# Performance work log

Measured on AMD Instinct MI355X. Metric: run time of the kernel, lower is better.

## Reference

```python
import jax, jax.numpy as jnp
import numpy as np

N_HEADS = 16
D_HEAD = 64
QUERY_DIM = 1024
CONTEXT_DIM = 1024
INNER = N_HEADS * D_HEAD


def setup_inputs() -> dict:
    key = jax.random.key(0)
    ks = jax.random.split(key, 7)
    B, Nq, Nk = 4, 1024, 1024
    x = jax.random.normal(ks[0], (B, Nq, QUERY_DIM), dtype=jnp.float32)
    context = jax.random.normal(ks[1], (B, Nk, CONTEXT_DIM), dtype=jnp.float32)
    s_q = 1.0 / np.sqrt(QUERY_DIM)
    s_c = 1.0 / np.sqrt(CONTEXT_DIM)
    s_i = 1.0 / np.sqrt(INNER)
    Wq = jax.random.uniform(ks[2], (QUERY_DIM, INNER), jnp.float32, -s_q, s_q)
    Wk = jax.random.uniform(ks[3], (CONTEXT_DIM, INNER), jnp.float32, -s_c, s_c)
    Wv = jax.random.uniform(ks[4], (CONTEXT_DIM, INNER), jnp.float32, -s_c, s_c)
    Wo = jax.random.uniform(ks[5], (INNER, QUERY_DIM), jnp.float32, -s_i, s_i)
    bo = jax.random.uniform(ks[6], (QUERY_DIM,), jnp.float32, -s_i, s_i)
    return {"x": x, "context": context, "Wq": Wq, "Wk": Wk, "Wv": Wv, "Wo": Wo, "bo": bo}


def reference(x, context, Wq, Wk, Wv, Wo, bo):
    B, Nq, _ = x.shape
    Nk = context.shape[1]
    scale = D_HEAD ** -0.5
    # project and split heads: [B, H, N, d]
    q = (x @ Wq).reshape(B, Nq, N_HEADS, D_HEAD).transpose(0, 2, 1, 3)
    k = (context @ Wk).reshape(B, Nk, N_HEADS, D_HEAD).transpose(0, 2, 1, 3)
    v = (context @ Wv).reshape(B, Nk, N_HEADS, D_HEAD).transpose(0, 2, 1, 3)
    scores = jnp.einsum("bhqd,bhkd->bhqk", q, k) * scale
    attn = jax.nn.softmax(scores, axis=-1)
    out = jnp.einsum("bhqk,bhkd->bhqd", attn, v)
    out = out.transpose(0, 2, 1, 3).reshape(B, Nq, INNER)
    return out @ Wo + bo
```

## Files before the change

### kernel.cpp

```cpp
#include <hip/hip_runtime.h>
#include <hip/hip_bf16.h>

#define BATCH 4
#define NQ 1024
#define NKK 1024
#define HD 1024
#define NHEADS 16

typedef __bf16 bf16x8 __attribute__((ext_vector_type(8)));
typedef float f32x4 __attribute__((ext_vector_type(4)));
typedef unsigned short u16;
typedef unsigned short u16x8 __attribute__((ext_vector_type(8)));
typedef unsigned int u32;

__device__ __forceinline__ u16 f2bf(float f) {
    union { __bf16 h; u16 u; } v;
    v.h = (__bf16)f;
    return v.u;
}

#define GLOAD16(gp, lp) \
    __builtin_amdgcn_global_load_lds((const __attribute__((address_space(1))) void*)(gp), \
                                     (__attribute__((address_space(3))) void*)(lp), 16, 0, 0)

#define MFMA16(a, b, c) __builtin_amdgcn_mfma_f32_16x16x32_bf16(a, b, c, 0, 0, 0)

__global__ __launch_bounds__(256) void prep_k(const float* __restrict__ x,
                                              const float* __restrict__ ctx,
                                              const float* __restrict__ w0,
                                              const float* __restrict__ w1,
                                              const float* __restrict__ w2,
                                              const float* __restrict__ w3,
                                              u16* __restrict__ ws,
                                              u16* __restrict__ Xb,
                                              u16* __restrict__ Cb) {
    const int tid = threadIdx.x;
    const int z = blockIdx.z;
    if (z >= 4) {
        const float* src = (z == 4) ? x : ctx;
        u16* dst = (z == 4) ? Xb : Cb;
        const int seg = blockIdx.y * 16 + blockIdx.x;
#pragma unroll
        for (int p = 0; p < 16; ++p) {
            const int i = seg * 4096 + p * 256 + tid;
            float4 v = ((const float4*)src)[i];
            ushort4 pk;
            pk.x = f2bf(v.x); pk.y = f2bf(v.y); pk.z = f2bf(v.z); pk.w = f2bf(v.w);
            ((ushort4*)dst)[i] = pk;
        }
        return;
    }
    const float* src = z == 0 ? w0 : z == 1 ? w1 : z == 2 ? w2 : w3;
    const float scl = (z == 0) ? 0.18033688011112042f : 1.0f;
    u16* dst = ws + (size_t)z * (1024u * 1024u);
    __shared__ u16 t[64][65];
    const int bx = blockIdx.x * 64;
    const int by = blockIdx.y * 64;
#pragma unroll
    for (int p = 0; p < 16; ++p) {
        int idx = p * 256 + tid;
        int r = idx >> 6, c = idx & 63;
        t[c][r] = f2bf(scl * src[(size_t)(by + r) * 1024 + bx + c]);
    }
    __syncthreads();
#pragma unroll
    for (int p = 0; p < 16; ++p) {
        int idx = p * 256 + tid;
        int r = idx >> 6, c = idx & 63;
        dst[(size_t)(bx + r) * 1024 + by + c] = t[r][c];
    }
}

__global__ __launch_bounds__(512) void gemm_qkv(const u16* __restrict__ Xb,
                                                const u16* __restrict__ Cb,
                                                const u16* __restrict__ WqT,
                                                const u16* __restrict__ WkT,
                                                const u16* __restrict__ WvT,
                                                u16* __restrict__ Qb,
                                                u16* __restrict__ Kb,
                                                u16* __restrict__ VTb) {
    const int bid = blockIdx.x;
    const int swz = (bid & 7) * 96 + (bid >> 3);
    const int z = swz >> 8;
    const int rem = swz & 255;
    const int m0 = (rem >> 3) * 128;
    const int n0 = (rem & 7) * 128;

    const u16* __restrict__ A  = (z == 0) ? Xb : Cb;
    const u16* __restrict__ BT = (z == 0) ? WqT : (z == 1) ? WkT : WvT;

    __shared__ __align__(16) u16 Asm[128 * 64];
    __shared__ __align__(16) u16 Bsm[128 * 64];

    const int tid = threadIdx.x, lane = tid & 63, wv = tid >> 6;
    const int wm = wv >> 2, wn = wv & 3;
    const int lr = lane & 15, lg = lane >> 4;
    const int lx = lr & 7;
    const int M = BATCH * NQ, N = HD, K = HD;

    f32x4 acc[4][2];
#pragma unroll
    for (int i = 0; i < 4; ++i)
#pragma unroll
        for (int j = 0; j < 2; ++j) acc[i][j] = (f32x4)(0.0f);

    for (int kt = 0; kt < K; kt += 64) {
        __syncthreads();
#pragma unroll
        for (int i = 0; i < 2; ++i) {
            const int cb = (wv * 2 + i) * 64;
            const int s = cb + lane;
            const int row = s >> 3, cg = (s & 7) ^ (row & 7);
            GLOAD16(A + (size_t)(m0 + row) * K + kt + cg * 8, &Asm[cb * 8]);
            GLOAD16(BT + (size_t)(n0 + row) * K + kt + cg * 8, &Bsm[cb * 8]);
        }
        __syncthreads();
        bf16x8 af[4][2], bfr[2][2];
#pragma unroll
        for (int m = 0; m < 4; ++m)
#pragma unroll
            for (int kk = 0; kk < 2; ++kk)
                af[m][kk] = *(const bf16x8*)&Asm[((wm * 64 + m * 16 + lr) * 8 +
                                                 ((kk * 4 + lg) ^ lx)) * 8];
#pragma unroll
        for (int n = 0; n < 2; ++n)
#pragma unroll
            for (int kk = 0; kk < 2; ++kk)
                bfr[n][kk] = *(const bf16x8*)&Bsm[((wn * 32 + n * 16 + lr) * 8 +
                                                  ((kk * 4 + lg) ^ lx)) * 8];
#pragma unroll
        for (int kk = 0; kk < 2; ++kk)
#pragma unroll
            for (int m = 0; m < 4; ++m)
#pragma unroll
                for (int n = 0; n < 2; ++n)
                    acc[m][n] = MFMA16(af[m][kk], bfr[n][kk], acc[m][n]);
    }

    if (z < 2) {
        u16* __restrict__ C = (z == 0) ? Qb : Kb;
#pragma unroll
        for (int m = 0; m < 4; ++m)
#pragma unroll
            for (int n = 0; n < 2; ++n) {
                const int col = n0 + wn * 32 + n * 16 + lr;
                const int rb = m0 + wm * 64 + m * 16 + lg * 4;
#pragma unroll
                for (int r = 0; r < 4; ++r)
                    C[(size_t)(rb + r) * N + col] = f2bf(acc[m][n][r]);
            }
    } else {
#pragma unroll
        for (int m = 0; m < 4; ++m)
#pragma unroll
            for (int n = 0; n < 2; ++n) {
                const int col = n0 + wn * 32 + n * 16 + lr;
                const int rb = m0 + wm * 64 + m * 16 + lg * 4;
                ushort4 pk;
                pk.x = f2bf(acc[m][n][0]);
                pk.y = f2bf(acc[m][n][1]);
                pk.z = f2bf(acc[m][n][2]);
                pk.w = f2bf(acc[m][n][3]);
                *(ushort4*)&VTb[(size_t)col * M + rb] = pk;
            }
    }
}

__global__ __launch_bounds__(512) void gemm_out(const u16* __restrict__ A,
                                                const u16* __restrict__ BT,
                                                const float* __restrict__ bias,
                                                float* __restrict__ C) {
    const int bid = blockIdx.x;
    const int swz = (bid & 7) * 32 + (bid >> 3);
    const int m0 = (swz >> 3) * 128;
    const int n0 = (swz & 7) * 128;

    __shared__ __align__(16) u16 Asm[128 * 64];
    __shared__ __align__(16) u16 Bsm[128 * 64];

    const int tid = threadIdx.x, lane = tid & 63, wv = tid >> 6;
    const int wm = wv >> 2, wn = wv & 3;
    const int lr = lane & 15, lg = lane >> 4;
    const int lx = lr & 7;
    const int N = HD, K = HD;

    f32x4 acc[4][2];
#pragma unroll
    for (int i = 0; i < 4; ++i)
#pragma unroll
        for (int j = 0; j < 2; ++j) acc[i][j] = (f32x4)(0.0f);

    for (int kt = 0; kt < K; kt += 64) {
        __syncthreads();
#pragma unroll
        for (int i = 0; i < 2; ++i) {
            const int cb = (wv * 2 + i) * 64;
            const int s = cb + lane;
            const int row = s >> 3, cg = (s & 7) ^ (row & 7);
            GLOAD16(A + (size_t)(m0 + row) * K + kt + cg * 8, &Asm[cb * 8]);
            GLOAD16(BT + (size_t)(n0 + row) * K + kt + cg * 8, &Bsm[cb * 8]);
        }
        __syncthreads();
        bf16x8 af[4][2], bfr[2][2];
#pragma unroll
        for (int m = 0; m < 4; ++m)
#pragma unroll
            for (int kk = 0; kk < 2; ++kk)
                af[m][kk] = *(const bf16x8*)&Asm[((wm * 64 + m * 16 + lr) * 8 +
                                                 ((kk * 4 + lg) ^ lx)) * 8];
#pragma unroll
        for (int n = 0; n < 2; ++n)
#pragma unroll
            for (int kk = 0; kk < 2; ++kk)
                bfr[n][kk] = *(const bf16x8*)&Bsm[((wn * 32 + n * 16 + lr) * 8 +
                                                  ((kk * 4 + lg) ^ lx)) * 8];
#pragma unroll
        for (int kk = 0; kk < 2; ++kk)
#pragma unroll
            for (int m = 0; m < 4; ++m)
#pragma unroll
                for (int n = 0; n < 2; ++n)
                    acc[m][n] = MFMA16(af[m][kk], bfr[n][kk], acc[m][n]);
    }

#pragma unroll
    for (int m = 0; m < 4; ++m)
#pragma unroll
        for (int n = 0; n < 2; ++n) {
            const int col = n0 + wn * 32 + n * 16 + lr;
            const int rb = m0 + wm * 64 + m * 16 + lg * 4;
            const float bv = bias[col];
#pragma unroll
            for (int r = 0; r < 4; ++r)
                C[(size_t)(rb + r) * N + col] = acc[m][n][r] + bv;
        }
}

__global__ __launch_bounds__(256) void attn_k(const u16* __restrict__ Q,
                                              const u16* __restrict__ Kp,
                                              const u16* __restrict__ VT,
                                              u16* __restrict__ AO) {
    __shared__ __align__(16) u16 Ksm[2][64 * 64];
    __shared__ __align__(16) u16 Vsm[2][64 * 64];
    __shared__ __align__(16) u16 Psm[4][16 * 64];

    const int tid = threadIdx.x, lane = tid & 63, wv = tid >> 6;
    const int lr = lane & 15, lg = lane >> 4;

    const int swz = (blockIdx.x & 7) * 128 + (blockIdx.x >> 3);
    const int bh = swz >> 4;
    const int b = bh >> 4, h = bh & 15;
    const int q0 = (swz & 15) * 64 + wv * 16;
    const int lx = lr & 7;

    bf16x8 qf[2];
#pragma unroll
    for (int ks = 0; ks < 2; ++ks)
        qf[ks] = *(const bf16x8*)&Q[(size_t)(b * NQ + q0 + lr) * HD +
                                    h * 64 + ks * 32 + lg * 8];

    bf16x8 onesf;
#pragma unroll
    for (int i = 0; i < 8; ++i) onesf[i] = (__bf16)1.0f;

    const int kbase = b * NKK, vrow0 = h * 64;
    auto stageKV = [&](int kt, int bufsel) {
#pragma unroll
        for (int i = 0; i < 2; ++i) {
            const int cb = (wv * 2 + i) * 64;
            const int s = cb + lane;
            const int row = s >> 3;
            const int cg = (s & 7) ^ (row & 7);
            GLOAD16(Kp + (size_t)(kbase + kt + row) * HD + h * 64 + cg * 8,
                    &Ksm[bufsel][cb * 8]);
            GLOAD16(VT + (size_t)(vrow0 + row) * (BATCH * NKK) + kbase + kt + cg * 8,
                    &Vsm[bufsel][cb * 8]);
        }
    };

    f32x4 osum = (f32x4)(0.0f);
    f32x4 o[4];
#pragma unroll
    for (int n = 0; n < 4; ++n) o[n] = (f32x4)(0.0f);

    stageKV(0, 0);
    __syncthreads();
    int cur = 0;

    for (int t = 0; t < NKK / 64; ++t) {
        if (t + 1 < NKK / 64) stageKV((t + 1) * 64, cur ^ 1);
        const u16* Ks = &Ksm[cur][0];
        const u16* Vs = &Vsm[cur][0];

        f32x4 s[4];
#pragma unroll
        for (int n = 0; n < 4; ++n) s[n] = (f32x4)(0.0f);
        __builtin_amdgcn_s_setprio(1);
#pragma unroll
        for (int n = 0; n < 4; ++n) {
            bf16x8 kf0 = *(const bf16x8*)&Ks[(n * 16 + lr) * 64 + (lg ^ lx) * 8];
            bf16x8 kf1 = *(const bf16x8*)&Ks[(n * 16 + lr) * 64 + ((lg | 4) ^ lx) * 8];
            s[n] = MFMA16(kf0, qf[0], s[n]);
            s[n] = MFMA16(kf1, qf[1], s[n]);
        }
        __builtin_amdgcn_s_setprio(0);

        u16* P = &Psm[wv][0];
#pragma unroll
        for (int n = 0; n < 4; ++n) {
            const float p0 = exp2f(s[n][0]);
            const float p1 = exp2f(s[n][1]);
            const float p2 = exp2f(s[n][2]);
            const float p3 = exp2f(s[n][3]);
            ushort4 pk;
            pk.x = f2bf(p0); pk.y = f2bf(p1); pk.z = f2bf(p2); pk.w = f2bf(p3);
            const int ch = (2 * n + (lg >> 1)) ^ lx;
            *(ushort4*)&P[lr * 64 + ch * 8 + (lg & 1) * 4] = pk;
        }

#pragma unroll
        for (int ks = 0; ks < 2; ++ks) {
            bf16x8 pa = *(const bf16x8*)&P[lr * 64 + (((ks * 4 + lg) ^ lx)) * 8];
            __builtin_amdgcn_s_setprio(1);
#pragma unroll
            for (int n = 0; n < 4; ++n) {
                bf16x8 vf = *(const bf16x8*)&Vs[(n * 16 + lr) * 64 + (((ks * 4 + lg) ^ lx)) * 8];
                o[n] = MFMA16(pa, vf, o[n]);
            }
            osum = MFMA16(pa, onesf, osum);
            __builtin_amdgcn_s_setprio(0);
        }
        __syncthreads();
        cur ^= 1;
    }

    float rs[4];
#pragma unroll
    for (int r = 0; r < 4; ++r) rs[r] = 1.0f / osum[r];

#pragma unroll
    for (int n = 0; n < 4; ++n)
#pragma unroll
        for (int r = 0; r < 4; ++r) {
            const float val = o[n][r] * rs[r];
            AO[(size_t)(b * NQ + q0 + lg * 4 + r) * HD +
               h * 64 + n * 16 + lr] = f2bf(val);
        }
}

extern "C" void kernel_launch(void* const* d_in, const int* in_sizes, int n_in,
                              void* d_out, int out_size, void* d_ws, size_t ws_size,
                              hipStream_t stream) {
    const float* x   = (const float*)d_in[0];
    const float* ctx = (const float*)d_in[1];
    const float* Wq  = (const float*)d_in[2];
    const float* Wk  = (const float*)d_in[3];
    const float* Wv  = (const float*)d_in[4];
    const float* Wo  = (const float*)d_in[5];
    const float* bo  = (const float*)d_in[6];

    u16* ws = (u16*)d_ws;
    const size_t MEG = 1024u * 1024u;
    u16* WqT = ws + 0 * MEG;
    u16* WkT = ws + 1 * MEG;
    u16* WvT = ws + 2 * MEG;
    u16* WoT = ws + 3 * MEG;
    u16* Xb  = ws + 4 * MEG;
    u16* Cb  = ws + 8 * MEG;
    u16* Qb  = ws + 12 * MEG;
    u16* Kb  = ws + 16 * MEG;
    u16* VTb = ws + 20 * MEG;
    u16* AOb = Xb;

    prep_k<<<dim3(16, 16, 6), 256, 0, stream>>>(x, ctx, Wq, Wk, Wv, Wo, ws, Xb, Cb);
    gemm_qkv<<<768, 512, 0, stream>>>(Xb, Cb, WqT, WkT, WvT, Qb, Kb, VTb);
    attn_k<<<1024, 256, 0, stream>>>(Qb, Kb, VTb, AOb);
    gemm_out<<<256, 512, 0, stream>>>(AOb, WoT, bo, (float*)d_out);
}
```

Measured before the change: 99.56 us.

## Rewrite QKV GEMM as 256x256 double-buffered pipelined kernel with interleaved loads

Replaces the 128x128 single-buffered QKV projection GEMM with a 256x256 tile kernel that keeps two K-stages in 128KB of dynamic LDS. Global-to-LDS loads for upcoming stages are split into halves and issued between MFMA phases, using explicit vmcnt waits, scheduling barriers and setprio. The three weight matrices are treated as one concatenated 3072-column B operand. The aim is to raise arithmetic intensity and hide load latency behind MFMA work. The cost is only 192 workgroups on a large-CU GPU, which risks poor occupancy and a tail effect.

```diff
diff --git a/kernel.cpp b/kernel.cpp
--- a/kernel.cpp
+++ b/kernel.cpp
@@ -24,6 +24,11 @@
                                      (__attribute__((address_space(3))) void*)(lp), 16, 0, 0)
 
 #define MFMA16(a, b, c) __builtin_amdgcn_mfma_f32_16x16x32_bf16(a, b, c, 0, 0, 0)
+
+#define SBAR()  do { __builtin_amdgcn_sched_barrier(0); __builtin_amdgcn_s_barrier(); \
+                     __builtin_amdgcn_sched_barrier(0); } while (0)
+#define VMW(N)  do { asm volatile("s_waitcnt vmcnt(" #N ")" ::: "memory"); \
+                     __builtin_amdgcn_sched_barrier(0); } while (0)
 
 __global__ __launch_bounds__(256) void prep_k(const float* __restrict__ x,
                                               const float* __restrict__ ctx,
@@ -71,96 +76,165 @@
     }
 }
 
-__global__ __launch_bounds__(512) void gemm_qkv(const u16* __restrict__ Xb,
-                                                const u16* __restrict__ Cb,
-                                                const u16* __restrict__ WqT,
-                                                const u16* __restrict__ WkT,
-                                                const u16* __restrict__ WvT,
-                                                u16* __restrict__ Qb,
-                                                u16* __restrict__ Kb,
-                                                u16* __restrict__ VTb) {
+template <int TB, int MH, int NH, class F>
+__device__ __forceinline__ void phase8(const u16* Asm, const u16* Bsm,
+                                       int wm, int wn, int lr, int lg, int lx,
+                                       f32x4 (&acc)[8][4], F&& stage) {
+    const u16* As = Asm + TB * 16384;
+    const u16* Bs = Bsm + TB * 16384;
+    bf16x8 af[4][2], bfr[2][2];
+#pragma unroll
+    for (int m = 0; m < 4; ++m)
+#pragma unroll
+        for (int kk = 0; kk < 2; ++kk)
+            af[m][kk] = *(const bf16x8*)&As[((wm * 128 + MH * 64 + m * 16 + lr) * 8 +
+                                            ((kk * 4 + lg) ^ lx)) * 8];
+#pragma unroll
+    for (int n = 0; n < 2; ++n)
+#pragma unroll
+        for (int kk = 0; kk < 2; ++kk)
+            bfr[n][kk] = *(const bf16x8*)&Bs[((wn * 64 + NH * 32 + n * 16 + lr) * 8 +
+                                             ((kk * 4 + lg) ^ lx)) * 8];
+    stage();
+    SBAR();
+    __builtin_amdgcn_s_setprio(1);
+#pragma unroll
+    for (int kk = 0; kk < 2; ++kk)
+#pragma unroll
+        for (int m = 0; m < 4; ++m)
+#pragma unroll
+            for (int n = 0; n < 2; ++n)
+                acc[MH * 4 + m][NH * 2 + n] =
+                    MFMA16(af[m][kk], bfr[n][kk], acc[MH * 4 + m][NH * 2 + n]);
+    __builtin_amdgcn_s_setprio(0);
+    __builtin_amdgcn_sched_barrier(0);
+}
+
+__global__ __launch_bounds__(512, 2) void gemm_qkv8(const u16* __restrict__ Xb,
+                                                    const u16* __restrict__ Cb,
+                                                    const u16* __restrict__ BT3,
+                                                    u16* __restrict__ Qb,
+                                                    u16* __restrict__ Kb,
+                                                    u16* __restrict__ VTb) {
+    extern __shared__ __align__(16) u16 dynlds[];
+    u16* Asm = dynlds;
+    u16* Bsm = dynlds + 2 * 16384;
+
     const int bid = blockIdx.x;
-    const int swz = (bid & 7) * 96 + (bid >> 3);
-    const int z = swz >> 8;
-    const int rem = swz & 255;
-    const int m0 = (rem >> 3) * 128;
-    const int n0 = (rem & 7) * 128;
-
-    const u16* __restrict__ A  = (z == 0) ? Xb : Cb;
-    const u16* __restrict__ BT = (z == 0) ? WqT : (z == 1) ? WkT : WvT;
-
-    __shared__ __align__(16) u16 Asm[128 * 64];
-    __shared__ __align__(16) u16 Bsm[128 * 64];
+    const int swz = (bid & 7) * 24 + (bid >> 3);
+    const int m0 = (swz / 12) * 256;
+    const int nblk = swz % 12;
+    const int n0g = nblk * 256;
+    const int z = n0g >> 10;
+    const int nc0 = n0g & 1023;
+
+    const u16* __restrict__ A = (z == 0) ? Xb : Cb;
 
     const int tid = threadIdx.x, lane = tid & 63, wv = tid >> 6;
     const int wm = wv >> 2, wn = wv & 3;
     const int lr = lane & 15, lg = lane >> 4;
     const int lx = lr & 7;
-    const int M = BATCH * NQ, N = HD, K = HD;
-
-    f32x4 acc[4][2];
-#pragma unroll
-    for (int i = 0; i < 4; ++i)
-#pragma unroll
-        for (int j = 0; j < 2; ++j) acc[i][j] = (f32x4)(0.0f);
-
-    for (int kt = 0; kt < K; kt += 64) {
-        __syncthreads();
-#pragma unroll
-        for (int i = 0; i < 2; ++i) {
-            const int cb = (wv * 2 + i) * 64;
-            const int s = cb + lane;
-            const int row = s >> 3, cg = (s & 7) ^ (row & 7);
-            GLOAD16(A + (size_t)(m0 + row) * K + kt + cg * 8, &Asm[cb * 8]);
-            GLOAD16(BT + (size_t)(n0 + row) * K + kt + cg * 8, &Bsm[cb * 8]);
-        }
-        __syncthreads();
-        bf16x8 af[4][2], bfr[2][2];
-#pragma unroll
-        for (int m = 0; m < 4; ++m)
-#pragma unroll
-            for (int kk = 0; kk < 2; ++kk)
-                af[m][kk] = *(const bf16x8*)&Asm[((wm * 64 + m * 16 + lr) * 8 +
-                                                 ((kk * 4 + lg) ^ lx)) * 8];
-#pragma unroll
-        for (int n = 0; n < 2; ++n)
-#pragma unroll
-            for (int kk = 0; kk < 2; ++kk)
-                bfr[n][kk] = *(const bf16x8*)&Bsm[((wn * 32 + n * 16 + lr) * 8 +
-                                                  ((kk * 4 + lg) ^ lx)) * 8];
-#pragma unroll
-        for (int kk = 0; kk < 2; ++kk)
-#pragma unroll
-            for (int m = 0; m < 4; ++m)
-#pragma unroll
-                for (int n = 0; n < 2; ++n)
-                    acc[m][n] = MFMA16(af[m][kk], bfr[n][kk], acc[m][n]);
-    }
+    const int M = BATCH * NQ;
+
+    auto stageA = [&](int T, int half) {
+        const int tb = T & 1;
+        const int kt = T * 64;
+#pragma unroll
+        for (int j = 0; j < 2; ++j) {
+            const int s = j * 512 + tid;
+            const int rp = s >> 3, pc = s & 7;
+            const int r = rp + (rp & 64) + half * 64;
+            const int cg = pc ^ (r & 7);
+            GLOAD16(A + (size_t)(m0 + r) * 1024 + kt + cg * 8,
+                    Asm + tb * 16384 + (r * 8 + pc) * 8);
+        }
+    };
+    auto stageB = [&](int T, int half) {
+        const int tb = T & 1;
+        const int kt = T * 64;
+#pragma unroll
+        for (int j = 0; j < 2; ++j) {
+            const int s = j * 512 + tid;
+            const int rp = s >> 3, pc = s & 7;
+            const int r = (rp & 31) + ((rp >> 5) << 6) + half * 32;
+            const int cg = pc ^ (r & 7);
+            GLOAD16(BT3 + (size_t)(n0g + r) * 1024 + kt + cg * 8,
+                    Bsm + tb * 16384 + (r * 8 + pc) * 8);
+        }
+    };
+
+    f32x4 acc[8][4];
+#pragma unroll
+    for (int i = 0; i < 8; ++i)
+#pragma unroll
+        for (int j = 0; j < 4; ++j) acc[i][j] = (f32x4)(0.0f);
+
+    stageA(0, 0); stageA(0, 1); stageB(0, 0); stageB(0, 1);
+    stageA(1, 0); stageA(1, 1); stageB(1, 0); stageB(1, 1);
+    VMW(8);
+    SBAR();
+
+    for (int i = 0; i < 7; ++i) {
+        const int t1 = 2 * i + 1, t2 = 2 * i + 2, t3 = 2 * i + 3;
+        phase8<0, 0, 0>(Asm, Bsm, wm, wn, lr, lg, lx, acc,
+                        [&] { if (i) stageA(t1, 1); });
+        SBAR();
+        phase8<0, 0, 1>(Asm, Bsm, wm, wn, lr, lg, lx, acc,
+                        [&] { if (i) stageB(t1, 1); });
+        SBAR();
+        phase8<0, 1, 0>(Asm, Bsm, wm, wn, lr, lg, lx, acc, [&] { stageA(t2, 0); });
+        SBAR();
+        phase8<0, 1, 1>(Asm, Bsm, wm, wn, lr, lg, lx, acc, [&] { stageB(t2, 0); });
+        VMW(4); SBAR();
+        phase8<1, 0, 0>(Asm, Bsm, wm, wn, lr, lg, lx, acc, [&] { stageA(t2, 1); });
+        SBAR();
+        phase8<1, 0, 1>(Asm, Bsm, wm, wn, lr, lg, lx, acc, [&] { stageB(t2, 1); });
+        SBAR();
+        phase8<1, 1, 0>(Asm, Bsm, wm, wn, lr, lg, lx, acc, [&] { stageA(t3, 0); });
+        SBAR();
+        phase8<1, 1, 1>(Asm, Bsm, wm, wn, lr, lg, lx, acc, [&] { stageB(t3, 0); });
+        VMW(4); SBAR();
+    }
+    phase8<0, 0, 0>(Asm, Bsm, wm, wn, lr, lg, lx, acc, [&] { stageA(15, 1); });
+    SBAR();
+    phase8<0, 0, 1>(Asm, Bsm, wm, wn, lr, lg, lx, acc, [&] { stageB(15, 1); });
+    SBAR();
+    phase8<0, 1, 0>(Asm, Bsm, wm, wn, lr, lg, lx, acc, [&] {});
+    SBAR();
+    phase8<0, 1, 1>(Asm, Bsm, wm, wn, lr, lg, lx, acc, [&] {});
+    VMW(0); SBAR();
+    phase8<1, 0, 0>(Asm, Bsm, wm, wn, lr, lg, lx, acc, [&] {});
+    SBAR();
+    phase8<1, 0, 1>(Asm, Bsm, wm, wn, lr, lg, lx, acc, [&] {});
+    SBAR();
+    phase8<1, 1, 0>(Asm, Bsm, wm, wn, lr, lg, lx, acc, [&] {});
+    SBAR();
+    phase8<1, 1, 1>(Asm, Bsm, wm, wn, lr, lg, lx, acc, [&] {});
 
     if (z < 2) {
         u16* __restrict__ C = (z == 0) ? Qb : Kb;
 #pragma unroll
-        for (int m = 0; m < 4; ++m)
-#pragma unroll
-            for (int n = 0; n < 2; ++n) {
-                const int col = n0 + wn * 32 + n * 16 + lr;
-                const int rb = m0 + wm * 64 + m * 16 + lg * 4;
+        for (int mf = 0; mf < 8; ++mf)
+#pragma unroll
+            for (int nf = 0; nf < 4; ++nf) {
+                const int col = nc0 + wn * 64 + nf * 16 + lr;
+                const int rb = m0 + wm * 128 + mf * 16 + lg * 4;
 #pragma unroll
                 for (int r = 0; r < 4; ++r)
-                    C[(size_t)(rb + r) * N + col] = f2bf(acc[m][n][r]);
+                    C[(size_t)(rb + r) * HD + col] = f2bf(acc[mf][nf][r]);
             }
     } else {
 #pragma unroll
-        for (int m = 0; m < 4; ++m)
-#pragma unroll
-            for (int n = 0; n < 2; ++n) {
-                const int col = n0 + wn * 32 + n * 16 + lr;
-                const int rb = m0 + wm * 64 + m * 16 + lg * 4;
+        for (int mf = 0; mf < 8; ++mf)
+#pragma unroll
+            for (int nf = 0; nf < 4; ++nf) {
+                const int col = nc0 + wn * 64 + nf * 16 + lr;
+                const int rb = m0 + wm * 128 + mf * 16 + lg * 4;
                 ushort4 pk;
-                pk.x = f2bf(acc[m][n][0]);
-                pk.y = f2bf(acc[m][n][1]);
-                pk.z = f2bf(acc[m][n][2]);
-                pk.w = f2bf(acc[m][n][3]);
+                pk.x = f2bf(acc[mf][nf][0]);
+                pk.y = f2bf(acc[mf][nf][1]);
+                pk.z = f2bf(acc[mf][nf][2]);
+                pk.w = f2bf(acc[mf][nf][3]);
                 *(ushort4*)&VTb[(size_t)col * M + rb] = pk;
             }
     }
@@ -361,9 +435,7 @@
 
     u16* ws = (u16*)d_ws;
     const size_t MEG = 1024u * 1024u;
-    u16* WqT = ws + 0 * MEG;
-    u16* WkT = ws + 1 * MEG;
-    u16* WvT = ws + 2 * MEG;
+    u16* WT3 = ws + 0 * MEG;
     u16* WoT = ws + 3 * MEG;
     u16* Xb  = ws + 4 * MEG;
     u16* Cb  = ws + 8 * MEG;
@@ -372,8 +444,11 @@
     u16* VTb = ws + 20 * MEG;
     u16* AOb = Xb;
 
+    hipFuncSetAttribute((const void*)gemm_qkv8,
+                        hipFuncAttributeMaxDynamicSharedMemorySize, 131072);
+
     prep_k<<<dim3(16, 16, 6), 256, 0, stream>>>(x, ctx, Wq, Wk, Wv, Wo, ws, Xb, Cb);
-    gemm_qkv<<<768, 512, 0, stream>>>(Xb, Cb, WqT, WkT, WvT, Qb, Kb, VTb);
+    gemm_qkv8<<<192, 512, 131072, stream>>>(Xb, Cb, WT3, Qb, Kb, VTb);
     attn_k<<<1024, 256, 0, stream>>>(Qb, Kb, VTb, AOb);
     gemm_out<<<256, 512, 0, stream>>>(AOb, WoT, bo, (float*)d_out);
 }
```

Result: slower. 107.4 us (+7.9%).
